# Optimization experiments

Hardware: AMD Instinct MI355X
Metric: run time of the kernel (lower is better)

Reference implementation:

```python
import jax, jax.numpy as jnp
import numpy as np

H, W, C = 80, 80, 64
R = 1.0  # rbf bandwidth (init kwarg r)


def setup_inputs() -> dict:
    key = jax.random.key(0)
    X = jax.random.normal(key, (H, W, C), dtype=jnp.float32)
    return {"X": X}


def reference(X):
    Hh, Ww, Cc = X.shape
    N = Hh * Ww

    # ---- coordinate similarity Ad (vectorized form of the O(N^2) loop) ----
    gr, gc = jnp.meshgrid(jnp.arange(Hh, dtype=X.dtype),
                          jnp.arange(Ww, dtype=X.dtype), indexing='ij')
    rf = gr.reshape(N)  # row coordinate i // W
    cf = gc.reshape(N)  # col coordinate i % W
    # squared euclidean distance between pixel coordinates, [N, N]
    d2 = (rf[:, None] - rf[None, :]) ** 2 + (cf[:, None] - cf[None, :]) ** 2
    Ad = jnp.exp(-d2 / (2.0 * R * R))
    # the python loop only fills i != j, so the diagonal stays 0
    Ad = Ad * (1.0 - jnp.eye(N, dtype=Ad.dtype))
    Ad = Ad / jnp.sum(Ad, axis=-1, keepdims=True)

    # ---- feature similarity As ----
    nodes = X.reshape(N, Cc)                      # [N, C]
    As = jax.nn.softmax(nodes @ nodes.T, axis=-1)  # [N, N], row softmax
    avg = jnp.mean(As, axis=-1, keepdims=True)     # per-row mean
    As = jnp.where(As < avg, jnp.zeros((), As.dtype), As)
    return Ad, As
```

## Files before the change

### kernel.cpp

```cpp
#include <hip/hip_runtime.h>

#define HH 80
#define NN 6400
#define CC 64
#define THR (1.0f / 6400.0f)

typedef _Float16 f16x8 __attribute__((ext_vector_type(8)));
typedef float float4v __attribute__((ext_vector_type(4)));

__global__ __launch_bounds__(256) void prep_kernel(
    const float* __restrict__ X,
    _Float16* __restrict__ Xhi, _Float16* __restrict__ Xlo,
    float* __restrict__ norms, float* __restrict__ denom,
    int* __restrict__ nmax)
{
    const int id = blockIdx.x * 256 + threadIdx.x;
    const float x = X[id];
    const _Float16 h = (_Float16)x;
    const float lo = x - (float)h;
    Xhi[id] = h;
    Xlo[id] = (_Float16)lo;

    float s = x * x;
#pragma unroll
    for (int m = 1; m < 64; m <<= 1) s += __shfl_xor(s, m, 64);
    const int lane = threadIdx.x & 63;
    if (lane == 0) {
        const int row = id >> 6;
        norms[row] = s;
        atomicMax(nmax, __float_as_int(s));
    }
    if (id < NN) denom[id] = 0.f;
}

__global__ __launch_bounds__(256) void pass1_kernel(
    const _Float16* __restrict__ Xhi, const _Float16* __restrict__ Xlo,
    const float* __restrict__ norms, const int* __restrict__ nmaxp,
    float* __restrict__ denom)
{
    const int tid = threadIdx.x;
    const int wave = tid >> 6, lane = tid & 63;
    const int q = lane >> 4, n16 = lane & 15;
    const int i0 = blockIdx.x * 256 + wave * 64;
    const int j0 = blockIdx.y * 256;
    const float nmax = __int_as_float(*nmaxp);

    f16x8 Ah[4][2], Al[4][2];
#pragma unroll
    for (int rt = 0; rt < 4; rt++) {
        const int row = i0 + rt * 16 + n16;
#pragma unroll
        for (int c = 0; c < 2; c++) {
            const int off = row * CC + c * 32 + q * 8;
            Ah[rt][c] = *(const f16x8*)(Xhi + off);
            Al[rt][c] = *(const f16x8*)(Xlo + off);
        }
    }
    float mh[4][4];
#pragma unroll
    for (int rt = 0; rt < 4; rt++)
#pragma unroll
        for (int r = 0; r < 4; r++)
            mh[rt][r] = sqrtf(norms[i0 + rt * 16 + q * 4 + r] * nmax);

    float cs[4][4];
#pragma unroll
    for (int rt = 0; rt < 4; rt++)
#pragma unroll
        for (int r = 0; r < 4; r++) cs[rt][r] = 0.f;

    for (int ct = 0; ct < 16; ct++) {
        const int col = j0 + ct * 16 + n16;
        f16x8 Bh[2], Bl[2];
#pragma unroll
        for (int c = 0; c < 2; c++) {
            const int off = col * CC + c * 32 + q * 8;
            Bh[c] = *(const f16x8*)(Xhi + off);
            Bl[c] = *(const f16x8*)(Xlo + off);
        }
#pragma unroll
        for (int rt = 0; rt < 4; rt++) {
            float4v acc = {0.f, 0.f, 0.f, 0.f};
#pragma unroll
            for (int c = 0; c < 2; c++) {
                acc = __builtin_amdgcn_mfma_f32_16x16x32_f16(Al[rt][c], Bh[c], acc, 0, 0, 0);
                acc = __builtin_amdgcn_mfma_f32_16x16x32_f16(Ah[rt][c], Bl[c], acc, 0, 0, 0);
                acc = __builtin_amdgcn_mfma_f32_16x16x32_f16(Ah[rt][c], Bh[c], acc, 0, 0, 0);
            }
#pragma unroll
            for (int r = 0; r < 4; r++)
                cs[rt][r] += __expf(acc[r] - mh[rt][r]);
        }
    }
#pragma unroll
    for (int rt = 0; rt < 4; rt++)
#pragma unroll
        for (int r = 0; r < 4; r++) {
            float v = cs[rt][r];
            v += __shfl_xor(v, 1, 64);
            v += __shfl_xor(v, 2, 64);
            v += __shfl_xor(v, 4, 64);
            v += __shfl_xor(v, 8, 64);
            if (n16 == 0)
                atomicAdd(&denom[i0 + rt * 16 + q * 4 + r], v);
        }
}

__global__ __launch_bounds__(256) void pass2_kernel(
    const _Float16* __restrict__ Xhi, const _Float16* __restrict__ Xlo,
    const float* __restrict__ norms, const int* __restrict__ nmaxp,
    const float* __restrict__ denom,
    float* __restrict__ Ad, float* __restrict__ As)
{
    __shared__ float Stab[HH];
    __shared__ float sMh[256], sRden[256], sRec[256];
    __shared__ int   sRC[256];
    const int tid = threadIdx.x;
    const int i0 = blockIdx.x * 256;
    const int j0 = blockIdx.y * 64;

    if (tid < HH) {
        float s = 0.f;
        for (int k = 0; k < HH; k++) {
            const float d = (float)(tid - k);
            s += __expf(-0.5f * d * d);
        }
        Stab[tid] = s;
    }
    __syncthreads();
    {
        const int i = i0 + tid;
        const float nmax = __int_as_float(*nmaxp);
        sMh[tid] = sqrtf(norms[i] * nmax);
        sRden[tid] = 1.0f / denom[i];
        const int r = i / HH, c = i - r * HH;
        sRec[tid] = 1.0f / (Stab[r] * Stab[c] - 1.0f);
        sRC[tid] = (r << 8) | c;
    }
    __syncthreads();

    const int wave = tid >> 6, lane = tid & 63;
    const int q = lane >> 4, n16 = lane & 15;
    const int iw = i0 + wave * 64;

    f16x8 Ah[4][2], Al[4][2];
#pragma unroll
    for (int rt = 0; rt < 4; rt++) {
        const int row = iw + rt * 16 + n16;
#pragma unroll
        for (int c = 0; c < 2; c++) {
            const int off = row * CC + c * 32 + q * 8;
            Ah[rt][c] = *(const f16x8*)(Xhi + off);
            Al[rt][c] = *(const f16x8*)(Xlo + off);
        }
    }

    float4v acc[4][4];
#pragma unroll
    for (int rt = 0; rt < 4; rt++)
#pragma unroll
        for (int ct = 0; ct < 4; ct++)
            acc[rt][ct] = (float4v){0.f, 0.f, 0.f, 0.f};

#pragma unroll
    for (int ct = 0; ct < 4; ct++) {
        const int col = j0 + ct * 16 + n16;
        f16x8 Bh[2], Bl[2];
#pragma unroll
        for (int c = 0; c < 2; c++) {
            const int off = col * CC + c * 32 + q * 8;
            Bh[c] = *(const f16x8*)(Xhi + off);
            Bl[c] = *(const f16x8*)(Xlo + off);
        }
#pragma unroll
        for (int rt = 0; rt < 4; rt++) {
#pragma unroll
            for (int c = 0; c < 2; c++) {
                acc[rt][ct] = __builtin_amdgcn_mfma_f32_16x16x32_f16(Al[rt][c], Bh[c], acc[rt][ct], 0, 0, 0);
                acc[rt][ct] = __builtin_amdgcn_mfma_f32_16x16x32_f16(Ah[rt][c], Bl[c], acc[rt][ct], 0, 0, 0);
                acc[rt][ct] = __builtin_amdgcn_mfma_f32_16x16x32_f16(Ah[rt][c], Bh[c], acc[rt][ct], 0, 0, 0);
            }
        }
    }

    int rj[4], cj[4];
#pragma unroll
    for (int ct = 0; ct < 4; ct++) {
        const int j = j0 + ct * 16 + n16;
        rj[ct] = j / HH;
        cj[ct] = j - rj[ct] * HH;
    }
#pragma unroll
    for (int rt = 0; rt < 4; rt++) {
#pragma unroll
        for (int r = 0; r < 4; r++) {
            const int il = wave * 64 + rt * 16 + q * 4 + r;
            const int i = i0 + il;
            const float mhv = sMh[il], rden = sRden[il], rec = sRec[il];
            const int rc = sRC[il];
            const int ri = rc >> 8, ci = rc & 255;
            float* __restrict__ AsRow = As + (size_t)i * NN;
            float* __restrict__ AdRow = Ad + (size_t)i * NN;
#pragma unroll
            for (int ct = 0; ct < 4; ct++) {
                const int j = j0 + ct * 16 + n16;
                float e = __expf(acc[rt][ct][r] - mhv) * rden;
                if (e < THR) e = 0.f;
                AsRow[j] = e;
                const int dr = ri - rj[ct], dc = ci - cj[ct];
                const float d2 = (float)(dr * dr + dc * dc);
                float ad = __expf(-0.5f * d2) * rec;
                if (i == j) ad = 0.f;
                AdRow[j] = ad;
            }
        }
    }
}

extern "C" void kernel_launch(void* const* d_in, const int* in_sizes, int n_in,
                              void* d_out, int out_size, void* d_ws, size_t ws_size,
                              hipStream_t stream) {
    const float* X = (const float*)d_in[0];
    float* Ad = (float*)d_out;
    float* As = Ad + (size_t)NN * NN;

    char* w = (char*)d_ws;
    _Float16* Xhi = (_Float16*)(w);
    _Float16* Xlo = (_Float16*)(w + 819200);
    float* norms  = (float*)(w + 1638400);
    float* denom  = (float*)(w + 1664000);
    int*   nmax   = (int*)(w + 1689600);

    prep_kernel<<<dim3((NN * CC) / 256), dim3(256), 0, stream>>>(
        X, Xhi, Xlo, norms, denom, nmax);
    pass1_kernel<<<dim3(25, 25), dim3(256), 0, stream>>>(
        Xhi, Xlo, norms, nmax, denom);
    pass2_kernel<<<dim3(25, 100), dim3(256), 0, stream>>>(
        Xhi, Xlo, norms, nmax, denom, Ad, As);
}
```

Baseline: 450.6 us.

## Split pass2 into separate As and Ad kernels with vectorized row-contiguous stores

```diff
diff --git a/kernel.cpp b/kernel.cpp
--- a/kernel.cpp
+++ b/kernel.cpp
@@ -12,7 +12,7 @@
     const float* __restrict__ X,
     _Float16* __restrict__ Xhi, _Float16* __restrict__ Xlo,
     float* __restrict__ norms, float* __restrict__ denom,
-    int* __restrict__ nmax)
+    int* __restrict__ nmax, float* __restrict__ Stab)
 {
     const int id = blockIdx.x * 256 + threadIdx.x;
     const float x = X[id];
@@ -31,6 +31,16 @@
         atomicMax(nmax, __float_as_int(s));
     }
     if (id < NN) denom[id] = 0.f;
+
+    const int t = (int)threadIdx.x;
+    if (blockIdx.x == 0 && t < HH) {
+        float acc = 0.f;
+        for (int k = 0; k < HH; k++) {
+            const float d = (float)(t - k);
+            acc += __expf(-0.5f * d * d);
+        }
+        Stab[t] = acc;
+    }
 }
 
 __global__ __launch_bounds__(256) void pass1_kernel(
@@ -106,36 +116,20 @@
         }
 }
 
-__global__ __launch_bounds__(256) void pass2_kernel(
+__global__ __launch_bounds__(256) void as_kernel(
     const _Float16* __restrict__ Xhi, const _Float16* __restrict__ Xlo,
     const float* __restrict__ norms, const int* __restrict__ nmaxp,
-    const float* __restrict__ denom,
-    float* __restrict__ Ad, float* __restrict__ As)
-{
-    __shared__ float Stab[HH];
-    __shared__ float sMh[256], sRden[256], sRec[256];
-    __shared__ int   sRC[256];
+    const float* __restrict__ denom, float* __restrict__ As)
+{
+    __shared__ float sMh[256], sRden[256];
     const int tid = threadIdx.x;
     const int i0 = blockIdx.x * 256;
-    const int j0 = blockIdx.y * 64;
-
-    if (tid < HH) {
-        float s = 0.f;
-        for (int k = 0; k < HH; k++) {
-            const float d = (float)(tid - k);
-            s += __expf(-0.5f * d * d);
-        }
-        Stab[tid] = s;
-    }
-    __syncthreads();
+    const int j0 = blockIdx.y * 256;
     {
         const int i = i0 + tid;
         const float nmax = __int_as_float(*nmaxp);
         sMh[tid] = sqrtf(norms[i] * nmax);
         sRden[tid] = 1.0f / denom[i];
-        const int r = i / HH, c = i - r * HH;
-        sRec[tid] = 1.0f / (Stab[r] * Stab[c] - 1.0f);
-        sRC[tid] = (r << 8) | c;
     }
     __syncthreads();
 
@@ -143,78 +137,80 @@
     const int q = lane >> 4, n16 = lane & 15;
     const int iw = i0 + wave * 64;
 
-    f16x8 Ah[4][2], Al[4][2];
+    f16x8 Bh[4][2], Bl[4][2];
 #pragma unroll
     for (int rt = 0; rt < 4; rt++) {
         const int row = iw + rt * 16 + n16;
 #pragma unroll
         for (int c = 0; c < 2; c++) {
             const int off = row * CC + c * 32 + q * 8;
-            Ah[rt][c] = *(const f16x8*)(Xhi + off);
-            Al[rt][c] = *(const f16x8*)(Xlo + off);
-        }
-    }
-
-    float4v acc[4][4];
-#pragma unroll
-    for (int rt = 0; rt < 4; rt++)
-#pragma unroll
-        for (int ct = 0; ct < 4; ct++)
-            acc[rt][ct] = (float4v){0.f, 0.f, 0.f, 0.f};
-
-#pragma unroll
-    for (int ct = 0; ct < 4; ct++) {
-        const int col = j0 + ct * 16 + n16;
-        f16x8 Bh[2], Bl[2];
-#pragma unroll
-        for (int c = 0; c < 2; c++) {
-            const int off = col * CC + c * 32 + q * 8;
-            Bh[c] = *(const f16x8*)(Xhi + off);
-            Bl[c] = *(const f16x8*)(Xlo + off);
-        }
+            Bh[rt][c] = *(const f16x8*)(Xhi + off);
+            Bl[rt][c] = *(const f16x8*)(Xlo + off);
+        }
+    }
+    float mh[4], rd[4];
+#pragma unroll
+    for (int rt = 0; rt < 4; rt++) {
+        const int il = wave * 64 + rt * 16 + n16;
+        mh[rt] = sMh[il];
+        rd[rt] = sRden[il];
+    }
+
+    for (int ct = 0; ct < 16; ct++) {
+        const int jt = j0 + ct * 16;
+        f16x8 Ahh[2], All[2];
+#pragma unroll
+        for (int c = 0; c < 2; c++) {
+            const int off = (jt + n16) * CC + c * 32 + q * 8;
+            Ahh[c] = *(const f16x8*)(Xhi + off);
+            All[c] = *(const f16x8*)(Xlo + off);
+        }
+        float4v acc[4];
+#pragma unroll
+        for (int rt = 0; rt < 4; rt++) acc[rt] = (float4v){0.f, 0.f, 0.f, 0.f};
 #pragma unroll
         for (int rt = 0; rt < 4; rt++) {
 #pragma unroll
             for (int c = 0; c < 2; c++) {
-                acc[rt][ct] = __builtin_amdgcn_mfma_f32_16x16x32_f16(Al[rt][c], Bh[c], acc[rt][ct], 0, 0, 0);
-                acc[rt][ct] = __builtin_amdgcn_mfma_f32_16x16x32_f16(Ah[rt][c], Bl[c], acc[rt][ct], 0, 0, 0);
-                acc[rt][ct] = __builtin_amdgcn_mfma_f32_16x16x32_f16(Ah[rt][c], Bh[c], acc[rt][ct], 0, 0, 0);
+                acc[rt] = __builtin_amdgcn_mfma_f32_16x16x32_f16(All[c], Bh[rt][c], acc[rt], 0, 0, 0);
+                acc[rt] = __builtin_amdgcn_mfma_f32_16x16x32_f16(Ahh[c], Bl[rt][c], acc[rt], 0, 0, 0);
+                acc[rt] = __builtin_amdgcn_mfma_f32_16x16x32_f16(Ahh[c], Bh[rt][c], acc[rt], 0, 0, 0);
             }
         }
-    }
-
-    int rj[4], cj[4];
-#pragma unroll
-    for (int ct = 0; ct < 4; ct++) {
-        const int j = j0 + ct * 16 + n16;
-        rj[ct] = j / HH;
-        cj[ct] = j - rj[ct] * HH;
-    }
-#pragma unroll
-    for (int rt = 0; rt < 4; rt++) {
-#pragma unroll
-        for (int r = 0; r < 4; r++) {
-            const int il = wave * 64 + rt * 16 + q * 4 + r;
-            const int i = i0 + il;
-            const float mhv = sMh[il], rden = sRden[il], rec = sRec[il];
-            const int rc = sRC[il];
-            const int ri = rc >> 8, ci = rc & 255;
-            float* __restrict__ AsRow = As + (size_t)i * NN;
-            float* __restrict__ AdRow = Ad + (size_t)i * NN;
-#pragma unroll
-            for (int ct = 0; ct < 4; ct++) {
-                const int j = j0 + ct * 16 + n16;
-                float e = __expf(acc[rt][ct][r] - mhv) * rden;
-                if (e < THR) e = 0.f;
-                AsRow[j] = e;
-                const int dr = ri - rj[ct], dc = ci - cj[ct];
-                const float d2 = (float)(dr * dr + dc * dc);
-                float ad = __expf(-0.5f * d2) * rec;
-                if (i == j) ad = 0.f;
-                AdRow[j] = ad;
+#pragma unroll
+        for (int rt = 0; rt < 4; rt++) {
+            float4v v;
+#pragma unroll
+            for (int r = 0; r < 4; r++) {
+                const float e = __expf(acc[rt][r] - mh[rt]) * rd[rt];
+                v[r] = (e < THR) ? 0.f : e;
             }
-        }
-    }
+            *(float4v*)(As + (size_t)(iw + rt * 16 + n16) * NN + jt + q * 4) = v;
+        }
+    }
+}
+
+__global__ __launch_bounds__(256) void ad_kernel(
+    const float* __restrict__ Stab, float* __restrict__ Ad)
+{
+    const int idx = blockIdx.x * 256 + threadIdx.x;
+    const int i = idx / 1600;
+    const int jq = (idx - i * 1600) * 4;
+    const int ri = i / HH, ci = i - ri * HH;
+    const int rj = jq / HH, cj0 = jq - rj * HH;
+    const float rec = 1.0f / (Stab[ri] * Stab[ci] - 1.0f);
+    const int dr = ri - rj;
+    const float dr2 = (float)(dr * dr);
+    float4v v;
+#pragma unroll
+    for (int r = 0; r < 4; r++) {
+        const int dc = ci - (cj0 + r);
+        const float d2 = dr2 + (float)(dc * dc);
+        float ad = __expf(-0.5f * d2) * rec;
+        if (i == jq + r) ad = 0.f;
+        v[r] = ad;
+    }
+    *(float4v*)(Ad + (size_t)idx * 4) = v;
 }
 
 extern "C" void kernel_launch(void* const* d_in, const int* in_sizes, int n_in,
@@ -230,11 +226,13 @@
     float* norms  = (float*)(w + 1638400);
     float* denom  = (float*)(w + 1664000);
     int*   nmax   = (int*)(w + 1689600);
+    float* Stab   = (float*)(w + 1689664);
 
     prep_kernel<<<dim3((NN * CC) / 256), dim3(256), 0, stream>>>(
-        X, Xhi, Xlo, norms, denom, nmax);
+        X, Xhi, Xlo, norms, denom, nmax, Stab);
     pass1_kernel<<<dim3(25, 25), dim3(256), 0, stream>>>(
         Xhi, Xlo, norms, nmax, denom);
-    pass2_kernel<<<dim3(25, 100), dim3(256), 0, stream>>>(
-        Xhi, Xlo, norms, nmax, denom, Ad, As);
-}
+    as_kernel<<<dim3(25, 25), dim3(256), 0, stream>>>(
+        Xhi, Xlo, norms, nmax, denom, As);
+    ad_kernel<<<dim3(NN * NN / 4 / 256), dim3(256), 0, stream>>>(Stab, Ad);
+}
```

Result: slower. 466.2 us, median of 2 (+3.5%).
